# Optimization experiments

Hardware: AMD Instinct MI355X
Metric: run time of the kernel (lower is better)

## Reference

```python
import jax, jax.numpy as jnp
import numpy as np

B, D_IN, UNITS, KFEAT = 2048, 2048, 1024, 49


def setup_inputs() -> dict:
    key = jax.random.key(0)
    ks = jax.random.split(key, 10)
    s = 0.02  # small init scale to keep sigmoids/tanh unsaturated
    return {
        "inputs": jax.random.normal(ks[0], (B, D_IN), jnp.float32),
        "h_tm": jax.random.normal(ks[1], (B, UNITS), jnp.float32),
        "m_tm": jax.random.normal(ks[2], (B, UNITS), jnp.float32),
        "v_seq": jax.random.normal(ks[3], (B, KFEAT, UNITS), jnp.float32),
        # gate weights stacked along output dim in order [f, i, o, g, a]
        "W_gates": jax.random.normal(ks[4], (UNITS, 5 * UNITS), jnp.float32) * s,
        "U_gates": jax.random.normal(ks[5], (D_IN, 5 * UNITS), jnp.float32) * s,
        "b_gates": jnp.zeros((5 * UNITS,), jnp.float32),
        "W_z": jax.random.normal(ks[6], (UNITS, KFEAT + 1), jnp.float32) * s,
        "U_z": jax.random.normal(ks[7], (UNITS, KFEAT + 1), jnp.float32) * s,
        "W_h": jax.random.normal(ks[8], (KFEAT + 1, 1), jnp.float32) * s,
    }


def reference(inputs, h_tm, m_tm, v_seq, W_gates, U_gates, b_gates, W_z, U_z, W_h):
    U = h_tm.shape[-1]
    # fused gate pre-activations: [B, 5U]
    z = h_tm @ W_gates + inputs @ U_gates + b_gates
    f, i, o, g, a = (z[:, j * U:(j + 1) * U] for j in range(5))
    ft = jax.nn.sigmoid(f)
    it = jax.nn.sigmoid(i)
    ot = jax.nn.sigmoid(o)
    gt = jax.nn.sigmoid(g)
    at = jnp.tanh(a)
    mt = m_tm * ft + it * at               # memory cell
    tanh_mt = jnp.tanh(mt)
    ht = ot * tanh_mt                      # hidden state
    st = gt * tanh_mt                      # visual sentinel
    # sentinel-augmented features: [B, K+1, U]
    v_expand = jnp.concatenate([v_seq, st[:, None, :]], axis=1)
    vtt = jnp.einsum('bku,uz->bkz', v_expand, W_z)   # [B, K+1, K+1]
    dtt = (ht @ U_z)[:, None, :]                     # broadcast over K+1 (K.repeat)
    zt = jnp.einsum('bkz,zo->bko', jnp.tanh(vtt + dtt), W_h)  # [B, K+1, 1]
    # NOTE: original uses keras softmax with default axis=-1 on a size-1 axis
    alpha_t = jax.nn.softmax(zt, axis=-1)            # [B, K+1, 1]
    ct = jnp.sum(alpha_t * v_expand, axis=1)         # batch_dot(axes=1) + squeeze
    return (ht + ct, ht, mt)
```

## Files before the change

### kernel.cpp

```cpp
#include <hip/hip_runtime.h>
#include <stdint.h>

#define BB   2048
#define DIN  2048
#define UU   1024
#define KF   49
#define GM   2048
#define GK   3072
#define GN   5120

#define BKS  32
#define SZB  18432

typedef __bf16  bf16x8 __attribute__((ext_vector_type(8)));
typedef float   f32x4  __attribute__((ext_vector_type(4)));

#define VL(dst, ptr) asm volatile("global_load_dwordx4 %0, %1, off" \
                                  : "=v"(dst) : "v"(ptr) : "memory")

static __device__ __forceinline__ unsigned short f2bf(float f) {
    union { float f; unsigned u; } x; x.f = f;
    unsigned u = x.u;
    unsigned r = (u + 0x7fffu + ((u >> 16) & 1u)) >> 16;
    return (unsigned short)r;
}

__global__ void prep(const float* __restrict__ h, const float* __restrict__ x,
                     const float* __restrict__ Wg, const float* __restrict__ Ug,
                     unsigned short* __restrict__ A, unsigned short* __restrict__ Wt) {
    __shared__ float t[32][36];
    if (blockIdx.x < 6144) {
        int idx = blockIdx.x * 256 + threadIdx.x;
        int b = idx / (GK / 4);
        int k = (idx % (GK / 4)) * 4;
        float4 v;
        if (k < UU) v = *(const float4*)(h + (size_t)b * UU + k);
        else        v = *(const float4*)(x + (size_t)b * DIN + (k - UU));
        ushort4 o;
        o.x = f2bf(v.x); o.y = f2bf(v.y); o.z = f2bf(v.z); o.w = f2bf(v.w);
        *(ushort4*)(A + (size_t)idx * 4) = o;
    } else {
        int bid2 = blockIdx.x - 6144;
        int k0 = (bid2 % (GK / 32)) * 32;
        int n0 = (bid2 / (GK / 32)) * 32;
        int r  = threadIdx.x >> 3;
        int cq = threadIdx.x & 7;
        int k = k0 + r;
        const float* src = (k < UU) ? (Wg + (size_t)k * GN) : (Ug + (size_t)(k - UU) * GN);
        *(float4*)&t[r][cq * 4] = *(const float4*)(src + n0 + cq * 4);
        __syncthreads();
        ushort4 o;
        o.x = f2bf(t[cq * 4 + 0][r]);
        o.y = f2bf(t[cq * 4 + 1][r]);
        o.z = f2bf(t[cq * 4 + 2][r]);
        o.w = f2bf(t[cq * 4 + 3][r]);
        *(ushort4*)(Wt + (size_t)(n0 + r) * GK + k0 + cq * 4) = o;
    }
}

__global__ __launch_bounds__(256, 2) void gemm_fused(
        const unsigned short* __restrict__ A, const unsigned short* __restrict__ Wt,
        const float* __restrict__ m_tm, const float* __restrict__ bg,
        const float* __restrict__ v_seq, float* __restrict__ out) {
    __shared__ __align__(16) char lds[3 * SZB];

    const int tid  = threadIdx.x;
    const int lane = tid & 63;
    const int wave = tid >> 6;
    const int wr = wave >> 1, wc = wave & 1;
    const int swz = (blockIdx.x & 7) * 64 + (blockIdx.x >> 3);
    const int brow  = (swz >> 5) * 128;
    const int ucol0 = (swz & 31) * 32;

    f32x4 acc[4][5];
#pragma unroll
    for (int m = 0; m < 4; m++)
#pragma unroll
        for (int g = 0; g < 5; g++) acc[m][g] = (f32x4){0.f, 0.f, 0.f, 0.f};

    const unsigned short* src[5];
    int ldsoff[5];
#pragma unroll
    for (int r = 0; r < 5; ++r) {
        if (r < 2) {
            int j = r * 256 + tid;
            src[r] = A + (size_t)(brow + (j >> 2)) * GK + (j & 3) * 8;
            ldsoff[r] = j * 16;
        } else {
            int j2 = (r < 4) ? (r - 2) * 256 + tid : 512 + (tid & 127);
            int g = j2 >> 7;
            int nn = (j2 >> 2) & 31;
            int c = j2 & 3;
            src[r] = Wt + ((size_t)g * UU + ucol0 + nn) * GK + c * 8;
            ldsoff[r] = 8192 + j2 * 16;
        }
    }

    int aoff[4], boff[5];
#pragma unroll
    for (int m = 0; m < 4; m++)
        aoff[m] = (wr * 64 + m * 16 + (lane & 15)) * 64 + (lane >> 4) * 16;
#pragma unroll
    for (int g = 0; g < 5; g++)
        boff[g] = 8192 + (g * 32 + wc * 16 + (lane & 15)) * 64 + (lane >> 4) * 16;

    auto STAGE = [&](int kstep, int bufb) {
        const int ko = kstep * BKS;
#pragma unroll
        for (int r = 0; r < 5; ++r)
            __builtin_amdgcn_global_load_lds(
                (const __attribute__((address_space(1))) void*)(src[r] + ko),
                (__attribute__((address_space(3))) void*)(lds + bufb + ldsoff[r]), 16, 0, 0);
    };
    auto COMPUTE = [&](int bufb) {
        bf16x8 af[4], bfr[5];
#pragma unroll
        for (int m = 0; m < 4; m++) af[m]  = *(const bf16x8*)(lds + bufb + aoff[m]);
#pragma unroll
        for (int g = 0; g < 5; g++) bfr[g] = *(const bf16x8*)(lds + bufb + boff[g]);
#pragma unroll
        for (int m = 0; m < 4; m++)
#pragma unroll
            for (int g = 0; g < 5; g++)
                acc[m][g] = __builtin_amdgcn_mfma_f32_16x16x32_bf16(af[m], bfr[g], acc[m][g], 0, 0, 0);
    };

    const float* vpa = v_seq + (size_t)(brow + (tid >> 2)) * (KF * UU) + ucol0 + (tid & 3) * 4;
    const float* vpc = vpa + (size_t)64 * KF * UU;
    f32x4 sa = {0,0,0,0}, sb = {0,0,0,0}, sc = {0,0,0,0}, sd = {0,0,0,0};
    f32x4 XA, XB, YA, YB;

    STAGE(0, 0);
    VL(XA, vpa);
    VL(XB, vpa + 16);
    STAGE(1, SZB);
    VL(YA, vpc);
    VL(YB, vpc + 16);
    asm volatile("s_waitcnt vmcnt(7)" ::: "memory");
    __builtin_amdgcn_s_barrier();
    __builtin_amdgcn_sched_barrier(0);

    int cb = 0;
    for (int tp = 0; tp < 47; ++tp) {
        {
            sa += XA; sb += XB;
            int sbuf = cb + 2 * SZB; if (sbuf >= 3 * SZB) sbuf -= 3 * SZB;
            STAGE(2 * tp + 2, sbuf);
            VL(XA, vpa + (size_t)(tp + 1) * UU);
            VL(XB, vpa + (size_t)(tp + 1) * UU + 16);
            COMPUTE(cb);
            asm volatile("s_waitcnt vmcnt(7)" ::: "memory");
            __builtin_amdgcn_s_barrier();
            __builtin_amdgcn_sched_barrier(0);
            cb += SZB; if (cb >= 3 * SZB) cb = 0;
        }
        {
            sc += YA; sd += YB;
            int sbuf = cb + 2 * SZB; if (sbuf >= 3 * SZB) sbuf -= 3 * SZB;
            STAGE(2 * tp + 3, sbuf);
            VL(YA, vpc + (size_t)(tp + 1) * UU);
            VL(YB, vpc + (size_t)(tp + 1) * UU + 16);
            COMPUTE(cb);
            asm volatile("s_waitcnt vmcnt(7)" ::: "memory");
            __builtin_amdgcn_s_barrier();
            __builtin_amdgcn_sched_barrier(0);
            cb += SZB; if (cb >= 3 * SZB) cb = 0;
        }
    }
    sa += XA; sb += XB;
    COMPUTE(cb);
    asm volatile("s_waitcnt vmcnt(0)" ::: "memory");
    __builtin_amdgcn_s_barrier();
    __builtin_amdgcn_sched_barrier(0);
    cb += SZB; if (cb >= 3 * SZB) cb = 0;
    sc += YA; sd += YB;
    COMPUTE(cb);

    {
        sa += *(const f32x4*)(vpa + (size_t)48 * UU);
        sb += *(const f32x4*)(vpa + (size_t)48 * UU + 16);
        sc += *(const f32x4*)(vpc + (size_t)48 * UU);
        sd += *(const f32x4*)(vpc + (size_t)48 * UU + 16);
    }

    float* lv = (float*)lds;
    {
        const int r = tid >> 2, c1 = (tid & 3) * 4;
        *(f32x4*)&lv[(size_t)r * 36 + c1]             = sa;
        *(f32x4*)&lv[(size_t)r * 36 + c1 + 16]        = sb;
        *(f32x4*)&lv[(size_t)(r + 64) * 36 + c1]      = sc;
        *(f32x4*)&lv[(size_t)(r + 64) * 36 + c1 + 16] = sd;
    }
    __syncthreads();

    const int ucol = ucol0 + wc * 16 + (lane & 15);
    const int lcol = wc * 16 + (lane & 15);
    const float b0 = bg[0 * UU + ucol];
    const float b1 = bg[1 * UU + ucol];
    const float b2 = bg[2 * UU + ucol];
    const float b3 = bg[3 * UU + ucol];
    const float b4 = bg[4 * UU + ucol];
    const int lr0 = wr * 64 + ((lane >> 4) << 2);
    float* out0 = out;
    float* out1 = out + (size_t)GM * UU;
    float* out2 = out + 2 * (size_t)GM * UU;
#pragma unroll
    for (int m = 0; m < 4; m++) {
#pragma unroll
        for (int j = 0; j < 4; j++) {
            const int lrow = lr0 + m * 16 + j;
            const int row  = brow + lrow;
            const size_t idx = (size_t)row * UU + ucol;
            const float vs  = lv[(size_t)lrow * 36 + lcol];
            const float mtm = m_tm[idx];
            const float f = acc[m][0][j] + b0;
            const float i = acc[m][1][j] + b1;
            const float o = acc[m][2][j] + b2;
            const float g = acc[m][3][j] + b3;
            const float a = acc[m][4][j] + b4;
            const float ft = 1.f / (1.f + __expf(-f));
            const float it = 1.f / (1.f + __expf(-i));
            const float ot = 1.f / (1.f + __expf(-o));
            const float gt = 1.f / (1.f + __expf(-g));
            const float at = tanhf(a);
            const float mtv = mtm * ft + it * at;
            const float tm  = tanhf(mtv);
            const float ht  = ot * tm;
            const float st  = gt * tm;
            out0[idx] = ht + vs + st;
            out1[idx] = ht;
            out2[idx] = mtv;
        }
    }
}

extern "C" void kernel_launch(void* const* d_in, const int* in_sizes, int n_in,
                              void* d_out, int out_size, void* d_ws, size_t ws_size,
                              hipStream_t stream) {
    (void)in_sizes; (void)n_in; (void)out_size; (void)ws_size;
    const float* inputs  = (const float*)d_in[0];
    const float* h_tm    = (const float*)d_in[1];
    const float* m_tm    = (const float*)d_in[2];
    const float* v_seq   = (const float*)d_in[3];
    const float* W_gates = (const float*)d_in[4];
    const float* U_gates = (const float*)d_in[5];
    const float* b_gates = (const float*)d_in[6];

    char* ws = (char*)d_ws;
    unsigned short* Abf = (unsigned short*)ws;
    unsigned short* Wt  = (unsigned short*)(ws + 12582912);
    float* out = (float*)d_out;

    hipLaunchKernelGGL(prep, dim3(6144 + (GK / 32) * (GN / 32)), dim3(256), 0, stream,
                       h_tm, inputs, W_gates, U_gates, Abf, Wt);
    hipLaunchKernelGGL(gemm_fused, dim3(512), dim3(256), 0, stream,
                       Abf, Wt, m_tm, b_gates, v_seq, out);
}
```

Before: 217.3 us.

## Halve GEMM row tile to 64, double buffering, launch twice the blocks

The fused gate GEMM block tile shrinks from 128 to 64 rows, so each block handles 64x(5x32) outputs and the grid doubles to 1024 blocks. The triple-buffered LDS pipeline becomes a double buffer with full vmcnt(0) waits, and launch bounds go to 4 blocks per CU for higher occupancy. The v_seq column-sum is restructured so each thread handles one row with 8 contiguous columns. The aim is better latency hiding and load balance, but the smaller tile reloads the weight matrix twice as often and the pipeline waits for all loads every step.

```diff
diff --git a/kernel.cpp b/kernel.cpp
--- a/kernel.cpp
+++ b/kernel.cpp
@@ -10,7 +10,7 @@
 #define GN   5120
 
 #define BKS  32
-#define SZB  18432
+#define SZB  14336
 
 typedef __bf16  bf16x8 __attribute__((ext_vector_type(8)));
 typedef float   f32x4  __attribute__((ext_vector_type(4)));
@@ -58,138 +58,120 @@
     }
 }
 
-__global__ __launch_bounds__(256, 2) void gemm_fused(
+__global__ __launch_bounds__(256, 4) void gemm_fused(
         const unsigned short* __restrict__ A, const unsigned short* __restrict__ Wt,
         const float* __restrict__ m_tm, const float* __restrict__ bg,
         const float* __restrict__ v_seq, float* __restrict__ out) {
-    __shared__ __align__(16) char lds[3 * SZB];
+    __shared__ __align__(16) char lds[2 * SZB];
 
     const int tid  = threadIdx.x;
     const int lane = tid & 63;
     const int wave = tid >> 6;
     const int wr = wave >> 1, wc = wave & 1;
-    const int swz = (blockIdx.x & 7) * 64 + (blockIdx.x >> 3);
-    const int brow  = (swz >> 5) * 128;
-    const int ucol0 = (swz & 31) * 32;
-
-    f32x4 acc[4][5];
-#pragma unroll
-    for (int m = 0; m < 4; m++)
+    const int brow  = (blockIdx.x >> 5) * 64;
+    const int ucol0 = (blockIdx.x & 31) * 32;
+
+    f32x4 acc[2][5];
+#pragma unroll
+    for (int m = 0; m < 2; m++)
 #pragma unroll
         for (int g = 0; g < 5; g++) acc[m][g] = (f32x4){0.f, 0.f, 0.f, 0.f};
 
-    const unsigned short* src[5];
-    int ldsoff[5];
-#pragma unroll
-    for (int r = 0; r < 5; ++r) {
-        if (r < 2) {
-            int j = r * 256 + tid;
+    const unsigned short* src[4];
+    int ldsoff[4];
+#pragma unroll
+    for (int r = 0; r < 4; ++r) {
+        if (r == 0) {
+            int j = tid;
             src[r] = A + (size_t)(brow + (j >> 2)) * GK + (j & 3) * 8;
             ldsoff[r] = j * 16;
         } else {
-            int j2 = (r < 4) ? (r - 2) * 256 + tid : 512 + (tid & 127);
+            int j2 = (r < 3) ? (r - 1) * 256 + tid : 512 + (tid & 127);
             int g = j2 >> 7;
             int nn = (j2 >> 2) & 31;
             int c = j2 & 3;
             src[r] = Wt + ((size_t)g * UU + ucol0 + nn) * GK + c * 8;
-            ldsoff[r] = 8192 + j2 * 16;
-        }
-    }
-
-    int aoff[4], boff[5];
-#pragma unroll
-    for (int m = 0; m < 4; m++)
-        aoff[m] = (wr * 64 + m * 16 + (lane & 15)) * 64 + (lane >> 4) * 16;
+            ldsoff[r] = 4096 + j2 * 16;
+        }
+    }
+
+    int aoff[2], boff[5];
+#pragma unroll
+    for (int m = 0; m < 2; m++)
+        aoff[m] = (wr * 32 + m * 16 + (lane & 15)) * 64 + (lane >> 4) * 16;
 #pragma unroll
     for (int g = 0; g < 5; g++)
-        boff[g] = 8192 + (g * 32 + wc * 16 + (lane & 15)) * 64 + (lane >> 4) * 16;
+        boff[g] = 4096 + (g * 32 + wc * 16 + (lane & 15)) * 64 + (lane >> 4) * 16;
 
     auto STAGE = [&](int kstep, int bufb) {
         const int ko = kstep * BKS;
 #pragma unroll
-        for (int r = 0; r < 5; ++r)
+        for (int r = 0; r < 4; ++r)
             __builtin_amdgcn_global_load_lds(
                 (const __attribute__((address_space(1))) void*)(src[r] + ko),
                 (__attribute__((address_space(3))) void*)(lds + bufb + ldsoff[r]), 16, 0, 0);
     };
     auto COMPUTE = [&](int bufb) {
-        bf16x8 af[4], bfr[5];
-#pragma unroll
-        for (int m = 0; m < 4; m++) af[m]  = *(const bf16x8*)(lds + bufb + aoff[m]);
+        bf16x8 af[2], bfr[5];
+#pragma unroll
+        for (int m = 0; m < 2; m++) af[m]  = *(const bf16x8*)(lds + bufb + aoff[m]);
 #pragma unroll
         for (int g = 0; g < 5; g++) bfr[g] = *(const bf16x8*)(lds + bufb + boff[g]);
 #pragma unroll
-        for (int m = 0; m < 4; m++)
+        for (int m = 0; m < 2; m++)
 #pragma unroll
             for (int g = 0; g < 5; g++)
                 acc[m][g] = __builtin_amdgcn_mfma_f32_16x16x32_bf16(af[m], bfr[g], acc[m][g], 0, 0, 0);
     };
 
-    const float* vpa = v_seq + (size_t)(brow + (tid >> 2)) * (KF * UU) + ucol0 + (tid & 3) * 4;
-    const float* vpc = vpa + (size_t)64 * KF * UU;
-    f32x4 sa = {0,0,0,0}, sb = {0,0,0,0}, sc = {0,0,0,0}, sd = {0,0,0,0};
-    f32x4 XA, XB, YA, YB;
+    const float* vp = v_seq + (size_t)(brow + (tid >> 2)) * (KF * UU)
+                    + ucol0 + (tid & 3) * 8;
+    f32x4 sa = {0,0,0,0}, sb = {0,0,0,0};
+    f32x4 XA, XB;
 
     STAGE(0, 0);
-    VL(XA, vpa);
-    VL(XB, vpa + 16);
-    STAGE(1, SZB);
-    VL(YA, vpc);
-    VL(YB, vpc + 16);
-    asm volatile("s_waitcnt vmcnt(7)" ::: "memory");
-    __builtin_amdgcn_s_barrier();
-    __builtin_amdgcn_sched_barrier(0);
-
-    int cb = 0;
-    for (int tp = 0; tp < 47; ++tp) {
-        {
-            sa += XA; sb += XB;
-            int sbuf = cb + 2 * SZB; if (sbuf >= 3 * SZB) sbuf -= 3 * SZB;
-            STAGE(2 * tp + 2, sbuf);
-            VL(XA, vpa + (size_t)(tp + 1) * UU);
-            VL(XB, vpa + (size_t)(tp + 1) * UU + 16);
-            COMPUTE(cb);
-            asm volatile("s_waitcnt vmcnt(7)" ::: "memory");
-            __builtin_amdgcn_s_barrier();
-            __builtin_amdgcn_sched_barrier(0);
-            cb += SZB; if (cb >= 3 * SZB) cb = 0;
-        }
-        {
-            sc += YA; sd += YB;
-            int sbuf = cb + 2 * SZB; if (sbuf >= 3 * SZB) sbuf -= 3 * SZB;
-            STAGE(2 * tp + 3, sbuf);
-            VL(YA, vpc + (size_t)(tp + 1) * UU);
-            VL(YB, vpc + (size_t)(tp + 1) * UU + 16);
-            COMPUTE(cb);
-            asm volatile("s_waitcnt vmcnt(7)" ::: "memory");
-            __builtin_amdgcn_s_barrier();
-            __builtin_amdgcn_sched_barrier(0);
-            cb += SZB; if (cb >= 3 * SZB) cb = 0;
-        }
-    }
-    sa += XA; sb += XB;
-    COMPUTE(cb);
+    VL(XA, vp);
     asm volatile("s_waitcnt vmcnt(0)" ::: "memory");
     __builtin_amdgcn_s_barrier();
     __builtin_amdgcn_sched_barrier(0);
-    cb += SZB; if (cb >= 3 * SZB) cb = 0;
-    sc += YA; sd += YB;
-    COMPUTE(cb);
-
-    {
-        sa += *(const f32x4*)(vpa + (size_t)48 * UU);
-        sb += *(const f32x4*)(vpa + (size_t)48 * UU + 16);
-        sc += *(const f32x4*)(vpc + (size_t)48 * UU);
-        sd += *(const f32x4*)(vpc + (size_t)48 * UU + 16);
-    }
-
+
+    int buf = 0;
+    for (int tp = 0; tp < 48; ++tp) {
+        {
+            STAGE(2 * tp + 1, buf ^ SZB);
+            VL(XB, vp + (size_t)tp * UU + 4);
+            COMPUTE(buf);
+            sa += XA;
+            asm volatile("s_waitcnt vmcnt(0)" ::: "memory");
+            __builtin_amdgcn_s_barrier();
+            __builtin_amdgcn_sched_barrier(0);
+            buf ^= SZB;
+        }
+        {
+            if (tp < 47) {
+                STAGE(2 * tp + 2, buf ^ SZB);
+                VL(XA, vp + (size_t)(tp + 1) * UU);
+            }
+            COMPUTE(buf);
+            sb += XB;
+            if (tp < 47) {
+                asm volatile("s_waitcnt vmcnt(0)" ::: "memory");
+                __builtin_amdgcn_s_barrier();
+                __builtin_amdgcn_sched_barrier(0);
+            }
+            buf ^= SZB;
+        }
+    }
+
+    sa += *(const f32x4*)(vp + (size_t)48 * UU);
+    sb += *(const f32x4*)(vp + (size_t)48 * UU + 4);
+
+    __syncthreads();
     float* lv = (float*)lds;
     {
-        const int r = tid >> 2, c1 = (tid & 3) * 4;
-        *(f32x4*)&lv[(size_t)r * 36 + c1]             = sa;
-        *(f32x4*)&lv[(size_t)r * 36 + c1 + 16]        = sb;
-        *(f32x4*)&lv[(size_t)(r + 64) * 36 + c1]      = sc;
-        *(f32x4*)&lv[(size_t)(r + 64) * 36 + c1 + 16] = sd;
+        const int r = tid >> 2, c = (tid & 3) * 8;
+        *(f32x4*)&lv[(size_t)r * 36 + c]     = sa;
+        *(f32x4*)&lv[(size_t)r * 36 + c + 4] = sb;
     }
     __syncthreads();
 
@@ -200,12 +182,12 @@
     const float b2 = bg[2 * UU + ucol];
     const float b3 = bg[3 * UU + ucol];
     const float b4 = bg[4 * UU + ucol];
-    const int lr0 = wr * 64 + ((lane >> 4) << 2);
+    const int lr0 = wr * 32 + ((lane >> 4) << 2);
     float* out0 = out;
     float* out1 = out + (size_t)GM * UU;
     float* out2 = out + 2 * (size_t)GM * UU;
 #pragma unroll
-    for (int m = 0; m < 4; m++) {
+    for (int m = 0; m < 2; m++) {
 #pragma unroll
         for (int j = 0; j < 4; j++) {
             const int lrow = lr0 + m * 16 + j;
@@ -253,6 +235,6 @@
 
     hipLaunchKernelGGL(prep, dim3(6144 + (GK / 32) * (GN / 32)), dim3(256), 0, stream,
                        h_tm, inputs, W_gates, U_gates, Abf, Wt);
-    hipLaunchKernelGGL(gemm_fused, dim3(512), dim3(256), 0, stream,
+    hipLaunchKernelGGL(gemm_fused, dim3(1024), dim3(256), 0, stream,
                        Abf, Wt, m_tm, b_gates, v_seq, out);
 }
```

After: 236.8 us. 9.0% more time.
